# Kernel tuning notes

Measured on AMD Instinct MI355X. Metric: run time of the kernel, lower is better.

The kernel has to match this reference:

```python
import jax, jax.numpy as jnp
import numpy as np

B, C, N, H = 4, 256, 1024, 8
D = C // H
EPS = 1e-5

def setup_inputs() -> dict:
    key = jax.random.key(0)
    ks = jax.random.split(key, 10)
    s = lambda k, shape: (jax.random.normal(k, shape, jnp.float32) * 0.02)
    return dict(
        node_embeds=jax.random.normal(ks[0], (B, C, N), jnp.float32),
        edge_embeds=jax.random.normal(ks[1], (B, N, N), jnp.float32),
        da_prior=jax.random.normal(ks[2], (B, N, C), jnp.float32),
        gamma=jnp.ones((C,), jnp.float32),
        beta=jnp.zeros((C,), jnp.float32),
        w_qkv=s(ks[3], (C, 3 * C)),            # Linear(node_dim, 3*node_dim), no bias
        w_proj=s(ks[4], (C, C)),
        b_proj=jnp.zeros((C,), jnp.float32),
        w_expand=s(ks[5], (H,)),               # Conv2d(1,H,1) weight (per-head scalar)
        b_expand=jnp.zeros((H,), jnp.float32),
        w_reduce=s(ks[6], (H,)),               # Conv2d(H,1,1) weight
        b_reduce=jnp.zeros((1,), jnp.float32),
        w_fc=s(ks[7], (1, C)),                 # Linear(edge_dim=1, node_dim)
        b_fc=jnp.zeros((C,), jnp.float32),
    )

def reference(node_embeds, edge_embeds, da_prior, gamma, beta, w_qkv,
              w_proj, b_proj, w_expand, b_expand, w_reduce, b_reduce, w_fc, b_fc):
    x = jnp.swapaxes(node_embeds, 1, 2)                       # [B,N,C]
    # einsum 'bnn,bnc->bnc': diagonal of edge matrix scales each node
    diag = jnp.diagonal(edge_embeds, axis1=1, axis2=2)        # [B,N]
    attned = diag[:, :, None] * x                             # [B,N,C]
    # einsum 'bnc,bca->bnc' with prior permuted [B,C,A]: multiply by sum over A
    prior_sum = da_prior.sum(axis=1)                          # [B,C]
    x = attned * prior_sum[:, None, :] + x                    # residual add
    # LayerNorm over channel dim
    mu = x.mean(-1, keepdims=True)
    var = x.var(-1, keepdims=True)
    ln = (x - mu) * jax.lax.rsqrt(var + EPS) * gamma + beta
    qkv = (ln @ w_qkv).reshape(B, N, 3, H, D)
    q = jnp.transpose(qkv[:, :, 0], (0, 2, 1, 3))             # [B,H,N,D]
    k = jnp.transpose(qkv[:, :, 1], (0, 2, 1, 3))
    v = jnp.transpose(qkv[:, :, 2], (0, 2, 1, 3))
    scale = D ** -0.5
    attn = jnp.einsum('bhnd,bhmd->bhnm', q, k) * scale        # [B,H,N,N]
    bias = edge_embeds[:, None] * w_expand[None, :, None, None] + b_expand[None, :, None, None]
    attn = attn + bias                                        # pre-softmax scores = residual
    a = jax.nn.softmax(attn, axis=-1)
    node = jnp.einsum('bhnm,bhmd->bnhd', a, v).reshape(B, N, C)
    # reduce conv over heads on (softmax + residual)
    edge = jnp.einsum('bhnm,h->bnm', a + attn, w_reduce) + b_reduce[0]  # [B,N,N]
    w = jax.nn.softmax(edge, axis=-1)
    wsum = (w * edge).sum(-1)                                 # [B,N]
    node = node + wsum[:, :, None] @ w_fc + b_fc              # fc: [B,N,1]@[1,C]
    node = node @ w_proj + b_proj
    return jnp.swapaxes(node, 1, 2), edge                     # ([B,C,N], [B,N,N])
```

## Files before the change

kernel.cpp:

```cpp
#include <hip/hip_runtime.h>
#include <math.h>

#define Bn 4
#define Cn 256
#define Nn 1024
#define Hn 8
#define Dn 32
#define BHND (Bn * Hn * Nn * Dn)
#define BHN  (Bn * Hn * Nn)

typedef short bf16x8 __attribute__((ext_vector_type(8)));
typedef float f32x4 __attribute__((ext_vector_type(4)));

__device__ inline unsigned f2bf_rn_bits(float x) {
  union { float f; unsigned u; } v; v.f = x;
  return (v.u + 0x7FFFu + ((v.u >> 16) & 1u)) >> 16;
}
__device__ inline float bfbits2f(unsigned b) {
  union { unsigned u; float f; } v; v.u = b << 16; return v.f;
}
__device__ inline void split_bf(float x, unsigned& hi, unsigned& lo) {
  hi = f2bf_rn_bits(x);
  lo = f2bf_rn_bits(x - bfbits2f(hi));
}
__device__ inline unsigned split_bf_trunc_pack(float x) {
  union { float f; unsigned u; } v; v.f = x;
  unsigned hi = v.u >> 16;
  union { unsigned u; float f; } hv; hv.u = hi << 16;
  union { float f; unsigned u; } r; r.f = x - hv.f;
  return hi | (r.u & 0xffff0000u);
}
__device__ inline void unpack_u32x8(const uint4& a, const uint4& b, bf16x8& hi, bf16x8& lo) {
  int4 h4, l4;
  h4.x = (int)((a.x & 0xffffu) | (a.y << 16));  l4.x = (int)((a.x >> 16) | (a.y & 0xffff0000u));
  h4.y = (int)((a.z & 0xffffu) | (a.w << 16));  l4.y = (int)((a.z >> 16) | (a.w & 0xffff0000u));
  h4.z = (int)((b.x & 0xffffu) | (b.y << 16));  l4.z = (int)((b.x >> 16) | (b.y & 0xffff0000u));
  h4.w = (int)((b.z & 0xffffu) | (b.w << 16));  l4.w = (int)((b.z >> 16) | (b.w & 0xffff0000u));
  hi = *(bf16x8*)&h4; lo = *(bf16x8*)&l4;
}

__global__ __launch_bounds__(256) void k_pre(const float* __restrict__ w,
                                             const float* __restrict__ dap,
                                             short* __restrict__ wt_h,
                                             short* __restrict__ wt_l,
                                             float* __restrict__ pp) {
  __shared__ float tile[32][33];
  int bi = blockIdx.x;
  if (bi < 32) {
    int b = bi >> 3, ch = bi & 7;
    int c = threadIdx.x;
    float s = 0.f;
    int n0 = ch * 128;
    for (int n = n0; n < n0 + 128; ++n) s += dap[(size_t)(b * Nn + n) * Cn + c];
    pp[(size_t)bi * Cn + c] = s;
  } else {
    int wi = bi - 32;
    int j0 = (wi >> 3) << 5;
    int k0 = (wi & 7) << 5;
    int tx = threadIdx.x & 31, ty = threadIdx.x >> 5;
#pragma unroll
    for (int i = 0; i < 4; ++i)
      tile[ty + i * 8][tx] = w[(size_t)(k0 + ty + i * 8) * 768 + j0 + tx];
    __syncthreads();
#pragma unroll
    for (int i = 0; i < 4; ++i) {
      float v = tile[tx][ty + i * 8];
      unsigned hb, lb; split_bf(v, hb, lb);
      wt_h[(size_t)(j0 + ty + i * 8) * 256 + k0 + tx] = (short)hb;
      wt_l[(size_t)(j0 + ty + i * 8) * 256 + k0 + tx] = (short)lb;
    }
  }
}

__global__ __launch_bounds__(256) void k_prep_ln(const float* __restrict__ ne,
                                                 const float* __restrict__ eg,
                                                 const float* __restrict__ pp,
                                                 const float* __restrict__ gamma,
                                                 const float* __restrict__ beta,
                                                 short* __restrict__ ln_h,
                                                 short* __restrict__ ln_l) {
  int bn = blockIdx.x;
  int b = bn >> 10, n = bn & 1023;
  int c = threadIdx.x;
  float x = ne[(size_t)(b * Cn + c) * Nn + n];
  float pr = 0.f;
#pragma unroll
  for (int ch = 0; ch < 8; ++ch) pr += pp[(size_t)(b * 8 + ch) * Cn + c];
  float dg = eg[(size_t)(b * Nn + n) * Nn + n];
  float x2 = x * (1.f + dg * pr);
  float s = x2, qq = x2 * x2;
#pragma unroll
  for (int off = 32; off >= 1; off >>= 1) {
    s += __shfl_xor(s, off);
    qq += __shfl_xor(qq, off);
  }
  __shared__ float ss[4], sq[4];
  if ((c & 63) == 0) { ss[c >> 6] = s; sq[c >> 6] = qq; }
  __syncthreads();
  s = ss[0] + ss[1] + ss[2] + ss[3];
  qq = sq[0] + sq[1] + sq[2] + sq[3];
  float mu = s * (1.f / 256.f);
  float var = qq * (1.f / 256.f) - mu * mu;
  float r = rsqrtf(var + 1e-5f);
  float v = (x2 - mu) * r * gamma[c] + beta[c];
  unsigned hb, lb; split_bf(v, hb, lb);
  ln_h[(size_t)bn * Cn + c] = (short)hb;
  ln_l[(size_t)bn * Cn + c] = (short)lb;
}

__global__ __launch_bounds__(256) void k_qkv_mfma(
    const short* __restrict__ ln_h, const short* __restrict__ ln_l,
    const short* __restrict__ wt_h, const short* __restrict__ wt_l,
    short* __restrict__ q_hi, short* __restrict__ q_lo,
    short* __restrict__ k_hi, short* __restrict__ k_lo,
    short* __restrict__ vt_hi, short* __restrict__ vt_lo) {
  __shared__ float ct[64][65];
  int m0 = blockIdx.x * 64;
  int j0 = blockIdx.y * 64;
  int t = threadIdx.x, wid = t >> 6, l = t & 63;
  int lr = l & 15, lq = l >> 4;
  f32x4 acc[4] = {};
  const short* ah_p = ln_h + (size_t)(m0 + wid * 16 + lr) * 256 + lq * 8;
  const short* al_p = ln_l + (size_t)(m0 + wid * 16 + lr) * 256 + lq * 8;
  const short* bh_p = wt_h + (size_t)(j0 + lr) * 256 + lq * 8;
  const short* bl_p = wt_l + (size_t)(j0 + lr) * 256 + lq * 8;
#pragma unroll 2
  for (int k0 = 0; k0 < 256; k0 += 32) {
    bf16x8 ah = *(const bf16x8*)&ah_p[k0];
    bf16x8 al = *(const bf16x8*)&al_p[k0];
#pragma unroll
    for (int js = 0; js < 4; ++js) {
      bf16x8 bh = *(const bf16x8*)&bh_p[js * 16 * 256 + k0];
      bf16x8 bl = *(const bf16x8*)&bl_p[js * 16 * 256 + k0];
      acc[js] = __builtin_amdgcn_mfma_f32_16x16x32_bf16(al, bh, acc[js], 0, 0, 0);
      acc[js] = __builtin_amdgcn_mfma_f32_16x16x32_bf16(ah, bl, acc[js], 0, 0, 0);
      acc[js] = __builtin_amdgcn_mfma_f32_16x16x32_bf16(ah, bh, acc[js], 0, 0, 0);
    }
  }
#pragma unroll
  for (int js = 0; js < 4; ++js)
#pragma unroll
    for (int reg = 0; reg < 4; ++reg)
      ct[wid * 16 + lq * 4 + reg][js * 16 + lr] = acc[js][reg];
  __syncthreads();
  int b = m0 >> 10, n0 = m0 & 1023;
  int three = j0 >> 8;
  const float scale = 0.17677669529663687f;
  if (three == 2) {
    int jl = t >> 2;
    int n4 = (t & 3) * 16;
    int rem = (j0 & 255) + jl;
    int h = rem >> 5, d = rem & 31;
    short hs[16], ls[16];
#pragma unroll
    for (int u = 0; u < 16; ++u) {
      unsigned hb, lb;
      split_bf(ct[n4 + u][jl], hb, lb);
      hs[u] = (short)hb; ls[u] = (short)lb;
    }
    size_t ob = ((size_t)(b * Hn + h) * Dn + d) * Nn + n0 + n4;
    *(uint4*)&vt_hi[ob] = *(uint4*)&hs[0];
    *(uint4*)&vt_hi[ob + 8] = *(uint4*)&hs[8];
    *(uint4*)&vt_lo[ob] = *(uint4*)&ls[0];
    *(uint4*)&vt_lo[ob + 8] = *(uint4*)&ls[8];
  } else {
    int m_l = t & 63, half = t >> 6;
    int rem = (j0 & 255) + half * 16;
    int h = rem >> 5, ddb = rem & 31;
    int n = n0 + m_l;
    float sc = (three == 0) ? 1.0f : scale;
    short* dh = three ? k_hi : q_hi;
    short* dl = three ? k_lo : q_lo;
    short hs[16], ls[16];
#pragma unroll
    for (int u = 0; u < 16; ++u) {
      unsigned hb, lb;
      split_bf(ct[m_l][half * 16 + u] * sc, hb, lb);
      hs[u] = (short)hb; ls[u] = (short)lb;
    }
    size_t base = ((size_t)((b * Hn + h) * Nn + n)) * Dn + ddb;
    *(uint4*)&dh[base] = *(uint4*)&hs[0];
    *(uint4*)&dh[base + 8] = *(uint4*)&hs[8];
    *(uint4*)&dl[base] = *(uint4*)&ls[0];
    *(uint4*)&dl[base + 8] = *(uint4*)&ls[8];
  }
}

__global__ __launch_bounds__(256, 4) void k_attn_core(
    const short* __restrict__ q_hi, const short* __restrict__ q_lo,
    const short* __restrict__ k_hi, const short* __restrict__ k_lo,
    const short* __restrict__ vt_hi, const short* __restrict__ vt_lo,
    const float* __restrict__ eg,
    const float* __restrict__ w_expand, const float* __restrict__ b_expand,
    float* __restrict__ o_part, float* __restrict__ l_part) {
  __shared__ short kh[64 * 40];
  __shared__ short kl[64 * 40];
  __shared__ short vth[32 * 72];
  __shared__ short vtl[32 * 72];
  __shared__ unsigned pbuf[4][16 * 68];

  int blk = blockIdx.x;
  int mh = blk & 1;
  int nt = (blk >> 1) & 15;
  int h = (blk >> 5) & 7;
  int b = blk >> 8;
  int n0 = nt * 64;
  int t = threadIdx.x, wid = t >> 6, l = t & 63;
  int lr = l & 15, lq = l >> 4;

  const float we = w_expand[h], be = b_expand[h];
  size_t bhb = (size_t)(b * Hn + h) * Nn * Dn;
  const short* khg = k_hi + bhb;
  const short* klg = k_lo + bhb;
  const short* vhg = vt_hi + bhb;
  const short* vlg = vt_lo + bhb;

  bf16x8 qhi, qlo;
  {
    size_t qoff = bhb + (size_t)(n0 + wid * 16 + lr) * Dn + lq * 8;
    qhi = *(const bf16x8*)&q_hi[qoff];
    qlo = *(const bf16x8*)&q_lo[qoff];
  }

  f32x4 O0 = {0.f, 0.f, 0.f, 0.f}, O1 = {0.f, 0.f, 0.f, 0.f};
  float rowsum[4] = {0.f, 0.f, 0.f, 0.f};
  int nrow = n0 + wid * 16 + lq * 4;

  for (int ms = 0; ms < 8; ++ms) {
    int m0 = mh * 512 + ms * 64;
    float eb[4][4];
#pragma unroll
    for (int reg = 0; reg < 4; ++reg) {
      const float* ep = &eg[(size_t)(b * Nn + nrow + reg) * Nn + m0 + lr];
#pragma unroll
      for (int msub = 0; msub < 4; ++msub) eb[msub][reg] = ep[msub * 16];
    }
    __syncthreads();
    {
      int row = t >> 2, c = (t & 3) * 8;
      *(uint4*)&kh[row * 40 + c] = *(const uint4*)&khg[(size_t)(m0 + row) * Dn + c];
      *(uint4*)&kl[row * 40 + c] = *(const uint4*)&klg[(size_t)(m0 + row) * Dn + c];
      int d = t >> 3, cm = (t & 7) * 8;
      *(uint4*)&vth[d * 72 + cm] = *(const uint4*)&vhg[(size_t)d * Nn + m0 + cm];
      *(uint4*)&vtl[d * 72 + cm] = *(const uint4*)&vlg[(size_t)d * Nn + m0 + cm];
    }
    __syncthreads();

#pragma unroll
    for (int msub = 0; msub < 4; ++msub) {
      int mrow = msub * 16 + lr;
      bf16x8 bh8 = *(bf16x8*)&kh[mrow * 40 + lq * 8];
      bf16x8 bl8 = *(bf16x8*)&kl[mrow * 40 + lq * 8];
      f32x4 sacc = {0.f, 0.f, 0.f, 0.f};
      sacc = __builtin_amdgcn_mfma_f32_16x16x32_bf16(qlo, bh8, sacc, 0, 0, 0);
      sacc = __builtin_amdgcn_mfma_f32_16x16x32_bf16(qhi, bl8, sacc, 0, 0, 0);
      sacc = __builtin_amdgcn_mfma_f32_16x16x32_bf16(qhi, bh8, sacc, 0, 0, 0);
#pragma unroll
      for (int reg = 0; reg < 4; ++reg) {
        float s = sacc[reg] + eb[msub][reg] * we + be;
        float e = __expf(s);
        rowsum[reg] += e;
        pbuf[wid][(lq * 4 + reg) * 68 + msub * 16 + lr] = split_bf_trunc_pack(e);
      }
    }

#pragma unroll
    for (int mw = 0; mw < 2; ++mw) {
      uint4 pa = *(uint4*)&pbuf[wid][lr * 68 + mw * 32 + lq * 8];
      uint4 pb = *(uint4*)&pbuf[wid][lr * 68 + mw * 32 + lq * 8 + 4];
      bf16x8 ahi, alo;
      unpack_u32x8(pa, pb, ahi, alo);
      {
        bf16x8 vh8 = *(bf16x8*)&vth[lr * 72 + mw * 32 + lq * 8];
        bf16x8 vl8 = *(bf16x8*)&vtl[lr * 72 + mw * 32 + lq * 8];
        O0 = __builtin_amdgcn_mfma_f32_16x16x32_bf16(alo, vh8, O0, 0, 0, 0);
        O0 = __builtin_amdgcn_mfma_f32_16x16x32_bf16(ahi, vl8, O0, 0, 0, 0);
        O0 = __builtin_amdgcn_mfma_f32_16x16x32_bf16(ahi, vh8, O0, 0, 0, 0);
      }
      {
        bf16x8 vh8 = *(bf16x8*)&vth[(16 + lr) * 72 + mw * 32 + lq * 8];
        bf16x8 vl8 = *(bf16x8*)&vtl[(16 + lr) * 72 + mw * 32 + lq * 8];
        O1 = __builtin_amdgcn_mfma_f32_16x16x32_bf16(alo, vh8, O1, 0, 0, 0);
        O1 = __builtin_amdgcn_mfma_f32_16x16x32_bf16(ahi, vl8, O1, 0, 0, 0);
        O1 = __builtin_amdgcn_mfma_f32_16x16x32_bf16(ahi, vh8, O1, 0, 0, 0);
      }
    }
  }

#pragma unroll
  for (int reg = 0; reg < 4; ++reg) {
#pragma unroll
    for (int off = 1; off < 16; off <<= 1)
      rowsum[reg] += __shfl_xor(rowsum[reg], off);
  }
  size_t pbase = (size_t)mh * BHND + bhb;
#pragma unroll
  for (int reg = 0; reg < 4; ++reg) {
    int n = nrow + reg;
    o_part[pbase + (size_t)n * Dn + lr] = O0[reg];
    o_part[pbase + (size_t)n * Dn + 16 + lr] = O1[reg];
    if (lr == 0)
      l_part[(size_t)mh * BHN + (size_t)(b * Hn + h) * Nn + n] = rowsum[reg];
  }
}

__global__ __launch_bounds__(256, 4) void k_edge_mfma(
    const short* __restrict__ q_hi, const short* __restrict__ q_lo,
    const short* __restrict__ k_hi, const short* __restrict__ k_lo,
    const float* __restrict__ eg, const float* __restrict__ l_part,
    const float* __restrict__ w_expand, const float* __restrict__ b_expand,
    const float* __restrict__ w_reduce, const float* __restrict__ b_reduce,
    float* __restrict__ edge_out, float* __restrict__ pl_part,
    float* __restrict__ pwe_part) {
  __shared__ short kh[64 * 40];
  __shared__ short kl[64 * 40];
  int blk = blockIdx.x;
  int mt = blk & 15;
  int nt = (blk >> 4) & 15;
  int b = blk >> 8;
  int n0 = nt * 64, m0 = mt * 64;
  int t = threadIdx.x, wid = t >> 6, l = t & 63;
  int lr = l & 15, lq = l >> 4;
  const float br = b_reduce[0];
  int nrow = n0 + wid * 16 + lq * 4;

  float eacc[4][4], ebias[4][4];
#pragma unroll
  for (int reg = 0; reg < 4; ++reg) {
    const float* ep = &eg[(size_t)(b * Nn + nrow + reg) * Nn + m0 + lr];
#pragma unroll
    for (int msub = 0; msub < 4; ++msub) {
      ebias[msub][reg] = ep[msub * 16];
      eacc[msub][reg] = br;
    }
  }

  for (int h = 0; h < Hn; ++h) {
    size_t bhb = (size_t)(b * Hn + h) * Nn * Dn;
    float we = w_expand[h], be = b_expand[h], wr = w_reduce[h];
    bf16x8 qhi, qlo;
    {
      size_t qoff = bhb + (size_t)(n0 + wid * 16 + lr) * Dn + lq * 8;
      qhi = *(const bf16x8*)&q_hi[qoff];
      qlo = *(const bf16x8*)&q_lo[qoff];
    }
    float invl[4];
#pragma unroll
    for (int reg = 0; reg < 4; ++reg) {
      size_t idx = (size_t)(b * Hn + h) * Nn + nrow + reg;
      invl[reg] = 1.0f / (l_part[idx] + l_part[BHN + idx]);
    }

    __syncthreads();
    {
      int row = t >> 2, c = (t & 3) * 8;
      *(uint4*)&kh[row * 40 + c] = *(const uint4*)&k_hi[bhb + (size_t)(m0 + row) * Dn + c];
      *(uint4*)&kl[row * 40 + c] = *(const uint4*)&k_lo[bhb + (size_t)(m0 + row) * Dn + c];
    }
    __syncthreads();
#pragma unroll
    for (int msub = 0; msub < 4; ++msub) {
      int mrow = msub * 16 + lr;
      bf16x8 bh8 = *(bf16x8*)&kh[mrow * 40 + lq * 8];
      bf16x8 bl8 = *(bf16x8*)&kl[mrow * 40 + lq * 8];
      f32x4 sacc = {0.f, 0.f, 0.f, 0.f};
      sacc = __builtin_amdgcn_mfma_f32_16x16x32_bf16(qlo, bh8, sacc, 0, 0, 0);
      sacc = __builtin_amdgcn_mfma_f32_16x16x32_bf16(qhi, bl8, sacc, 0, 0, 0);
      sacc = __builtin_amdgcn_mfma_f32_16x16x32_bf16(qhi, bh8, sacc, 0, 0, 0);
#pragma unroll
      for (int reg = 0; reg < 4; ++reg) {
        float s = sacc[reg] + ebias[msub][reg] * we + be;
        float p = __expf(s) * invl[reg];
        eacc[msub][reg] += wr * (p + s);
      }
    }
  }
#pragma unroll
  for (int msub = 0; msub < 4; ++msub)
#pragma unroll
    for (int reg = 0; reg < 4; ++reg)
      edge_out[(size_t)(b * Nn + nrow + reg) * Nn + m0 + msub * 16 + lr] = eacc[msub][reg];

  float pl[4] = {0.f, 0.f, 0.f, 0.f}, pw[4] = {0.f, 0.f, 0.f, 0.f};
#pragma unroll
  for (int msub = 0; msub < 4; ++msub)
#pragma unroll
    for (int reg = 0; reg < 4; ++reg) {
      float e = eacc[msub][reg];
      float x = __expf(e);
      pl[reg] += x;
      pw[reg] += x * e;
    }
#pragma unroll
  for (int reg = 0; reg < 4; ++reg) {
#pragma unroll
    for (int off = 1; off < 16; off <<= 1) {
      pl[reg] += __shfl_xor(pl[reg], off);
      pw[reg] += __shfl_xor(pw[reg], off);
    }
    if (lr == 0) {
      int idx = mt * (Bn * Nn) + b * Nn + nrow + reg;
      pl_part[idx] = pl[reg];
      pwe_part[idx] = pw[reg];
    }
  }
}

__global__ __launch_bounds__(256) void k_proj_gemm(const float* __restrict__ o_part,
                                                   const float* __restrict__ l_part,
                                                   const float* __restrict__ pl,
                                                   const float* __restrict__ pwe,
                                                   const float* __restrict__ wfc,
                                                   const float* __restrict__ bfc,
                                                   const float* __restrict__ wproj,
                                                   const float* __restrict__ bproj,
                                                   float* __restrict__ out) {
  __shared__ __align__(16) float at[16][68];
  __shared__ __align__(16) float bt[16][68];
  __shared__ float ct[64][65];
  __shared__ float wsm_s[64];
  int m0 = blockIdx.x * 64;
  int j0 = blockIdx.y * 64;
  int t = threadIdx.x;
  int tx = t & 15, ty = t >> 4;
  if (t < 64) {
    int m = m0 + t;
    float L = 0.f, Wv = 0.f;
#pragma unroll
    for (int mt = 0; mt < 16; ++mt) {
      L += pl[mt * (Bn * Nn) + m];
      Wv += pwe[mt * (Bn * Nn) + m];
    }
    wsm_s[t] = Wv / L;
  }
  __syncthreads();
  float4 acc[4] = {};
  for (int k0 = 0; k0 < 256; k0 += 16) {
    {
      int row = t >> 2, k4 = (t & 3) << 2;
      int m = m0 + row;
      int bb = m >> 10, n = m & 1023;
      int c = k0 + k4;
      int h = c >> 5, dd = c & 31;
      float wsm = wsm_s[row];
      size_t ob = ((size_t)(bb * Hn + h) * Nn + n) * Dn + dd;
      float4 oa = *(const float4*)&o_part[ob];
      float4 oc = *(const float4*)&o_part[BHND + ob];
      size_t sidx = (size_t)(bb * Hn + h) * Nn + n;
      float inv = 1.0f / (l_part[sidx] + l_part[BHN + sidx]);
      float4 a;
      a.x = (oa.x + oc.x) * inv + wsm * wfc[c + 0] + bfc[c + 0];
      a.y = (oa.y + oc.y) * inv + wsm * wfc[c + 1] + bfc[c + 1];
      a.z = (oa.z + oc.z) * inv + wsm * wfc[c + 2] + bfc[c + 2];
      a.w = (oa.w + oc.w) * inv + wsm * wfc[c + 3] + bfc[c + 3];
      at[k4 + 0][row] = a.x; at[k4 + 1][row] = a.y;
      at[k4 + 2][row] = a.z; at[k4 + 3][row] = a.w;
      int rb = t >> 4, jb = (t & 15) << 2;
      *(float4*)&bt[rb][jb] = *(const float4*)&wproj[(size_t)(k0 + rb) * 256 + j0 + jb];
    }
    __syncthreads();
#pragma unroll
    for (int kk = 0; kk < 16; ++kk) {
      float4 a4 = *(float4*)&at[kk][ty << 2];
      float4 b4 = *(float4*)&bt[kk][tx << 2];
      acc[0].x += a4.x * b4.x; acc[0].y += a4.x * b4.y; acc[0].z += a4.x * b4.z; acc[0].w += a4.x * b4.w;
      acc[1].x += a4.y * b4.x; acc[1].y += a4.y * b4.y; acc[1].z += a4.y * b4.z; acc[1].w += a4.y * b4.w;
      acc[2].x += a4.z * b4.x; acc[2].y += a4.z * b4.y; acc[2].z += a4.z * b4.z; acc[2].w += a4.z * b4.w;
      acc[3].x += a4.w * b4.x; acc[3].y += a4.w * b4.y; acc[3].z += a4.w * b4.z; acc[3].w += a4.w * b4.w;
    }
    __syncthreads();
  }
#pragma unroll
  for (int i = 0; i < 4; ++i) {
    ct[(ty << 2) + i][(tx << 2) + 0] = acc[i].x + bproj[j0 + (tx << 2) + 0];
    ct[(ty << 2) + i][(tx << 2) + 1] = acc[i].y + bproj[j0 + (tx << 2) + 1];
    ct[(ty << 2) + i][(tx << 2) + 2] = acc[i].z + bproj[j0 + (tx << 2) + 2];
    ct[(ty << 2) + i][(tx << 2) + 3] = acc[i].w + bproj[j0 + (tx << 2) + 3];
  }
  __syncthreads();
  int b = m0 >> 10, n0 = m0 & 1023;
  int n4 = t & 15, c0i = t >> 4;
#pragma unroll
  for (int u = 0; u < 4; ++u) {
    int ci = c0i + u * 16;
    float4 val = { ct[(n4 << 2) + 0][ci], ct[(n4 << 2) + 1][ci],
                   ct[(n4 << 2) + 2][ci], ct[(n4 << 2) + 3][ci] };
    *(float4*)&out[(size_t)(b * Cn + j0 + ci) * Nn + n0 + (n4 << 2)] = val;
  }
}

extern "C" void kernel_launch(void* const* d_in, const int* in_sizes, int n_in,
                              void* d_out, int out_size, void* d_ws, size_t ws_size,
                              hipStream_t stream) {
  (void)in_sizes; (void)n_in; (void)out_size; (void)ws_size;
  const float* node_embeds = (const float*)d_in[0];
  const float* edge_embeds = (const float*)d_in[1];
  const float* da_prior    = (const float*)d_in[2];
  const float* gamma       = (const float*)d_in[3];
  const float* beta        = (const float*)d_in[4];
  const float* w_qkv       = (const float*)d_in[5];
  const float* w_proj      = (const float*)d_in[6];
  const float* b_proj      = (const float*)d_in[7];
  const float* w_expand    = (const float*)d_in[8];
  const float* b_expand    = (const float*)d_in[9];
  const float* w_reduce    = (const float*)d_in[10];
  const float* b_reduce    = (const float*)d_in[11];
  const float* w_fc        = (const float*)d_in[12];
  const float* b_fc        = (const float*)d_in[13];
  float* out_node = (float*)d_out;
  float* out_edge = out_node + (size_t)Bn * Cn * Nn;

  const size_t M = 1048576;
  float* W = (float*)d_ws;
  short* ln_hi  = (short*)(W + M);
  short* ln_lo  = ln_hi + M;
  float* o_part = W;
  short* vt_hi  = (short*)(W + 2 * M);
  short* vt_lo  = vt_hi + M;
  short* q_hi   = (short*)(W + 3 * M);
  short* q_lo   = q_hi + M;
  short* k_hi   = q_hi + 2 * M;
  short* k_lo   = q_hi + 3 * M;
  float* ws_pp    = W + 5 * M;
  float* l_part   = ws_pp + Bn * 8 * Cn;
  float* pl_part  = l_part + 2 * BHN;
  float* pwe_part = pl_part + 16 * Bn * Nn;
  short* wt_hi    = (short*)(pwe_part + 16 * Bn * Nn);
  short* wt_lo    = wt_hi + 768 * 256;

  k_pre<<<dim3(224), dim3(256), 0, stream>>>(w_qkv, da_prior, wt_hi, wt_lo, ws_pp);
  k_prep_ln<<<dim3(Bn * Nn), dim3(256), 0, stream>>>(node_embeds, edge_embeds, ws_pp,
                                                     gamma, beta, ln_hi, ln_lo);
  k_qkv_mfma<<<dim3(64, 12), dim3(256), 0, stream>>>(ln_hi, ln_lo, wt_hi, wt_lo,
                                                     q_hi, q_lo, k_hi, k_lo,
                                                     vt_hi, vt_lo);
  k_attn_core<<<dim3(Bn * Hn * 16 * 2), dim3(256), 0, stream>>>(
      q_hi, q_lo, k_hi, k_lo, vt_hi, vt_lo, edge_embeds, w_expand, b_expand,
      o_part, l_part);
  k_edge_mfma<<<dim3(Bn * 16 * 16), dim3(256), 0, stream>>>(
      q_hi, q_lo, k_hi, k_lo, edge_embeds, l_part, w_expand, b_expand,
      w_reduce, b_reduce, out_edge, pl_part, pwe_part);
  k_proj_gemm<<<dim3(64, 4), dim3(256), 0, stream>>>(o_part, l_part, pl_part,
                                                     pwe_part, w_fc, b_fc,
                                                     w_proj, b_proj, out_node);
}
```

Before: 202.2 us.

## Stage QKV GEMM tiles in LDS and process two heads per attention block

The QKV GEMM now loads its A and B hi/lo tiles cooperatively into shared memory, prefetching the next k-slice into registers, so per-wave global loads of B are no longer repeated across waves. The attention core kernel now handles two heads per block, so each edge-bias tile read from global memory is reused for both heads. This halves the grid, relaxes launch bounds to 2 blocks per SM, and doubles per-block register state. The cost is fewer blocks for latency hiding and extra syncs.

```diff
diff --git a/kernel.cpp b/kernel.cpp
--- a/kernel.cpp
+++ b/kernel.cpp
@@ -114,29 +114,49 @@
     short* __restrict__ q_hi, short* __restrict__ q_lo,
     short* __restrict__ k_hi, short* __restrict__ k_lo,
     short* __restrict__ vt_hi, short* __restrict__ vt_lo) {
+  __shared__ short Ah[64 * 40];
+  __shared__ short Al[64 * 40];
+  __shared__ short Bh[64 * 40];
+  __shared__ short Bl[64 * 40];
   __shared__ float ct[64][65];
   int m0 = blockIdx.x * 64;
   int j0 = blockIdx.y * 64;
   int t = threadIdx.x, wid = t >> 6, l = t & 63;
   int lr = l & 15, lq = l >> 4;
   f32x4 acc[4] = {};
-  const short* ah_p = ln_h + (size_t)(m0 + wid * 16 + lr) * 256 + lq * 8;
-  const short* al_p = ln_l + (size_t)(m0 + wid * 16 + lr) * 256 + lq * 8;
-  const short* bh_p = wt_h + (size_t)(j0 + lr) * 256 + lq * 8;
-  const short* bl_p = wt_l + (size_t)(j0 + lr) * 256 + lq * 8;
-#pragma unroll 2
-  for (int k0 = 0; k0 < 256; k0 += 32) {
-    bf16x8 ah = *(const bf16x8*)&ah_p[k0];
-    bf16x8 al = *(const bf16x8*)&al_p[k0];
+  int row = t >> 2, ch = (t & 3) * 8;
+  const short* a_h_src = ln_h + (size_t)(m0 + row) * 256 + ch;
+  const short* a_l_src = ln_l + (size_t)(m0 + row) * 256 + ch;
+  const short* b_h_src = wt_h + (size_t)(j0 + row) * 256 + ch;
+  const short* b_l_src = wt_l + (size_t)(j0 + row) * 256 + ch;
+  uint4 vah = *(const uint4*)&a_h_src[0];
+  uint4 val = *(const uint4*)&a_l_src[0];
+  uint4 vbh = *(const uint4*)&b_h_src[0];
+  uint4 vbl = *(const uint4*)&b_l_src[0];
+  for (int it = 0; it < 8; ++it) {
+    __syncthreads();
+    *(uint4*)&Ah[row * 40 + ch] = vah;
+    *(uint4*)&Al[row * 40 + ch] = val;
+    *(uint4*)&Bh[row * 40 + ch] = vbh;
+    *(uint4*)&Bl[row * 40 + ch] = vbl;
+    __syncthreads();
+    int kn = ((it + 1) & 7) * 32;
+    vah = *(const uint4*)&a_h_src[kn];
+    val = *(const uint4*)&a_l_src[kn];
+    vbh = *(const uint4*)&b_h_src[kn];
+    vbl = *(const uint4*)&b_l_src[kn];
+    bf16x8 ah = *(bf16x8*)&Ah[(wid * 16 + lr) * 40 + lq * 8];
+    bf16x8 al8 = *(bf16x8*)&Al[(wid * 16 + lr) * 40 + lq * 8];
 #pragma unroll
     for (int js = 0; js < 4; ++js) {
-      bf16x8 bh = *(const bf16x8*)&bh_p[js * 16 * 256 + k0];
-      bf16x8 bl = *(const bf16x8*)&bl_p[js * 16 * 256 + k0];
-      acc[js] = __builtin_amdgcn_mfma_f32_16x16x32_bf16(al, bh, acc[js], 0, 0, 0);
+      bf16x8 bh = *(bf16x8*)&Bh[(js * 16 + lr) * 40 + lq * 8];
+      bf16x8 bl = *(bf16x8*)&Bl[(js * 16 + lr) * 40 + lq * 8];
+      acc[js] = __builtin_amdgcn_mfma_f32_16x16x32_bf16(al8, bh, acc[js], 0, 0, 0);
       acc[js] = __builtin_amdgcn_mfma_f32_16x16x32_bf16(ah, bl, acc[js], 0, 0, 0);
       acc[js] = __builtin_amdgcn_mfma_f32_16x16x32_bf16(ah, bh, acc[js], 0, 0, 0);
     }
   }
+  __syncthreads();
 #pragma unroll
   for (int js = 0; js < 4; ++js)
 #pragma unroll
@@ -186,7 +206,7 @@
   }
 }
 
-__global__ __launch_bounds__(256, 4) void k_attn_core(
+__global__ __launch_bounds__(256, 2) void k_attn_core(
     const short* __restrict__ q_hi, const short* __restrict__ q_lo,
     const short* __restrict__ k_hi, const short* __restrict__ k_lo,
     const short* __restrict__ vt_hi, const short* __restrict__ vt_lo,
@@ -202,28 +222,28 @@
   int blk = blockIdx.x;
   int mh = blk & 1;
   int nt = (blk >> 1) & 15;
-  int h = (blk >> 5) & 7;
-  int b = blk >> 8;
+  int hp = (blk >> 5) & 3;
+  int b = blk >> 7;
   int n0 = nt * 64;
   int t = threadIdx.x, wid = t >> 6, l = t & 63;
   int lr = l & 15, lq = l >> 4;
 
-  const float we = w_expand[h], be = b_expand[h];
-  size_t bhb = (size_t)(b * Hn + h) * Nn * Dn;
-  const short* khg = k_hi + bhb;
-  const short* klg = k_lo + bhb;
-  const short* vhg = vt_hi + bhb;
-  const short* vlg = vt_lo + bhb;
-
-  bf16x8 qhi, qlo;
-  {
-    size_t qoff = bhb + (size_t)(n0 + wid * 16 + lr) * Dn + lq * 8;
-    qhi = *(const bf16x8*)&q_hi[qoff];
-    qlo = *(const bf16x8*)&q_lo[qoff];
-  }
-
-  f32x4 O0 = {0.f, 0.f, 0.f, 0.f}, O1 = {0.f, 0.f, 0.f, 0.f};
-  float rowsum[4] = {0.f, 0.f, 0.f, 0.f};
+  float we[2], be[2];
+  size_t bhb[2];
+  bf16x8 qhi[2], qlo[2];
+#pragma unroll
+  for (int hh = 0; hh < 2; ++hh) {
+    int h = hp * 2 + hh;
+    we[hh] = w_expand[h]; be[hh] = b_expand[h];
+    bhb[hh] = (size_t)(b * Hn + h) * Nn * Dn;
+    size_t qoff = bhb[hh] + (size_t)(n0 + wid * 16 + lr) * Dn + lq * 8;
+    qhi[hh] = *(const bf16x8*)&q_hi[qoff];
+    qlo[hh] = *(const bf16x8*)&q_lo[qoff];
+  }
+
+  f32x4 O0[2] = {{0.f,0.f,0.f,0.f},{0.f,0.f,0.f,0.f}};
+  f32x4 O1[2] = {{0.f,0.f,0.f,0.f},{0.f,0.f,0.f,0.f}};
+  float rowsum[2][4] = {};
   int nrow = n0 + wid * 16 + lq * 4;
 
   for (int ms = 0; ms < 8; ++ms) {
@@ -235,72 +255,82 @@
 #pragma unroll
       for (int msub = 0; msub < 4; ++msub) eb[msub][reg] = ep[msub * 16];
     }
-    __syncthreads();
-    {
-      int row = t >> 2, c = (t & 3) * 8;
-      *(uint4*)&kh[row * 40 + c] = *(const uint4*)&khg[(size_t)(m0 + row) * Dn + c];
-      *(uint4*)&kl[row * 40 + c] = *(const uint4*)&klg[(size_t)(m0 + row) * Dn + c];
-      int d = t >> 3, cm = (t & 7) * 8;
-      *(uint4*)&vth[d * 72 + cm] = *(const uint4*)&vhg[(size_t)d * Nn + m0 + cm];
-      *(uint4*)&vtl[d * 72 + cm] = *(const uint4*)&vlg[(size_t)d * Nn + m0 + cm];
-    }
-    __syncthreads();
-
-#pragma unroll
-    for (int msub = 0; msub < 4; ++msub) {
-      int mrow = msub * 16 + lr;
-      bf16x8 bh8 = *(bf16x8*)&kh[mrow * 40 + lq * 8];
-      bf16x8 bl8 = *(bf16x8*)&kl[mrow * 40 + lq * 8];
-      f32x4 sacc = {0.f, 0.f, 0.f, 0.f};
-      sacc = __builtin_amdgcn_mfma_f32_16x16x32_bf16(qlo, bh8, sacc, 0, 0, 0);
-      sacc = __builtin_amdgcn_mfma_f32_16x16x32_bf16(qhi, bl8, sacc, 0, 0, 0);
-      sacc = __builtin_amdgcn_mfma_f32_16x16x32_bf16(qhi, bh8, sacc, 0, 0, 0);
-#pragma unroll
-      for (int reg = 0; reg < 4; ++reg) {
-        float s = sacc[reg] + eb[msub][reg] * we + be;
-        float e = __expf(s);
-        rowsum[reg] += e;
-        pbuf[wid][(lq * 4 + reg) * 68 + msub * 16 + lr] = split_bf_trunc_pack(e);
+#pragma unroll
+    for (int hh = 0; hh < 2; ++hh) {
+      __syncthreads();
+      {
+        int row = t >> 2, c = (t & 3) * 8;
+        const short* khg = k_hi + bhb[hh];
+        const short* klg = k_lo + bhb[hh];
+        const short* vhg = vt_hi + bhb[hh];
+        const short* vlg = vt_lo + bhb[hh];
+        *(uint4*)&kh[row * 40 + c] = *(const uint4*)&khg[(size_t)(m0 + row) * Dn + c];
+        *(uint4*)&kl[row * 40 + c] = *(const uint4*)&klg[(size_t)(m0 + row) * Dn + c];
+        int d = t >> 3, cm = (t & 7) * 8;
+        *(uint4*)&vth[d * 72 + cm] = *(const uint4*)&vhg[(size_t)d * Nn + m0 + cm];
+        *(uint4*)&vtl[d * 72 + cm] = *(const uint4*)&vlg[(size_t)d * Nn + m0 + cm];
       }
-    }
-
-#pragma unroll
-    for (int mw = 0; mw < 2; ++mw) {
-      uint4 pa = *(uint4*)&pbuf[wid][lr * 68 + mw * 32 + lq * 8];
-      uint4 pb = *(uint4*)&pbuf[wid][lr * 68 + mw * 32 + lq * 8 + 4];
-      bf16x8 ahi, alo;
-      unpack_u32x8(pa, pb, ahi, alo);
-      {
-        bf16x8 vh8 = *(bf16x8*)&vth[lr * 72 + mw * 32 + lq * 8];
-        bf16x8 vl8 = *(bf16x8*)&vtl[lr * 72 + mw * 32 + lq * 8];
-        O0 = __builtin_amdgcn_mfma_f32_16x16x32_bf16(alo, vh8, O0, 0, 0, 0);
-        O0 = __builtin_amdgcn_mfma_f32_16x16x32_bf16(ahi, vl8, O0, 0, 0, 0);
-        O0 = __builtin_amdgcn_mfma_f32_16x16x32_bf16(ahi, vh8, O0, 0, 0, 0);
+      __syncthreads();
+
+#pragma unroll
+      for (int msub = 0; msub < 4; ++msub) {
+        int mrow = msub * 16 + lr;
+        bf16x8 bh8 = *(bf16x8*)&kh[mrow * 40 + lq * 8];
+        bf16x8 bl8 = *(bf16x8*)&kl[mrow * 40 + lq * 8];
+        f32x4 sacc = {0.f, 0.f, 0.f, 0.f};
+        sacc = __builtin_amdgcn_mfma_f32_16x16x32_bf16(qlo[hh], bh8, sacc, 0, 0, 0);
+        sacc = __builtin_amdgcn_mfma_f32_16x16x32_bf16(qhi[hh], bl8, sacc, 0, 0, 0);
+        sacc = __builtin_amdgcn_mfma_f32_16x16x32_bf16(qhi[hh], bh8, sacc, 0, 0, 0);
+#pragma unroll
+        for (int reg = 0; reg < 4; ++reg) {
+          float s = sacc[reg] + eb[msub][reg] * we[hh] + be[hh];
+          float e = __expf(s);
+          rowsum[hh][reg] += e;
+          pbuf[wid][(lq * 4 + reg) * 68 + msub * 16 + lr] = split_bf_trunc_pack(e);
+        }
       }
-      {
-        bf16x8 vh8 = *(bf16x8*)&vth[(16 + lr) * 72 + mw * 32 + lq * 8];
-        bf16x8 vl8 = *(bf16x8*)&vtl[(16 + lr) * 72 + mw * 32 + lq * 8];
-        O1 = __builtin_amdgcn_mfma_f32_16x16x32_bf16(alo, vh8, O1, 0, 0, 0);
-        O1 = __builtin_amdgcn_mfma_f32_16x16x32_bf16(ahi, vl8, O1, 0, 0, 0);
-        O1 = __builtin_amdgcn_mfma_f32_16x16x32_bf16(ahi, vh8, O1, 0, 0, 0);
+
+#pragma unroll
+      for (int mw = 0; mw < 2; ++mw) {
+        uint4 pa = *(uint4*)&pbuf[wid][lr * 68 + mw * 32 + lq * 8];
+        uint4 pb = *(uint4*)&pbuf[wid][lr * 68 + mw * 32 + lq * 8 + 4];
+        bf16x8 ahi, alo;
+        unpack_u32x8(pa, pb, ahi, alo);
+        {
+          bf16x8 vh8 = *(bf16x8*)&vth[lr * 72 + mw * 32 + lq * 8];
+          bf16x8 vl8 = *(bf16x8*)&vtl[lr * 72 + mw * 32 + lq * 8];
+          O0[hh] = __builtin_amdgcn_mfma_f32_16x16x32_bf16(alo, vh8, O0[hh], 0, 0, 0);
+          O0[hh] = __builtin_amdgcn_mfma_f32_16x16x32_bf16(ahi, vl8, O0[hh], 0, 0, 0);
+          O0[hh] = __builtin_amdgcn_mfma_f32_16x16x32_bf16(ahi, vh8, O0[hh], 0, 0, 0);
+        }
+        {
+          bf16x8 vh8 = *(bf16x8*)&vth[(16 + lr) * 72 + mw * 32 + lq * 8];
+          bf16x8 vl8 = *(bf16x8*)&vtl[(16 + lr) * 72 + mw * 32 + lq * 8];
+          O1[hh] = __builtin_amdgcn_mfma_f32_16x16x32_bf16(alo, vh8, O1[hh], 0, 0, 0);
+          O1[hh] = __builtin_amdgcn_mfma_f32_16x16x32_bf16(ahi, vl8, O1[hh], 0, 0, 0);
+          O1[hh] = __builtin_amdgcn_mfma_f32_16x16x32_bf16(ahi, vh8, O1[hh], 0, 0, 0);
+        }
       }
     }
   }
 
 #pragma unroll
-  for (int reg = 0; reg < 4; ++reg) {
-#pragma unroll
-    for (int off = 1; off < 16; off <<= 1)
-      rowsum[reg] += __shfl_xor(rowsum[reg], off);
-  }
-  size_t pbase = (size_t)mh * BHND + bhb;
-#pragma unroll
-  for (int reg = 0; reg < 4; ++reg) {
-    int n = nrow + reg;
-    o_part[pbase + (size_t)n * Dn + lr] = O0[reg];
-    o_part[pbase + (size_t)n * Dn + 16 + lr] = O1[reg];
-    if (lr == 0)
-      l_part[(size_t)mh * BHN + (size_t)(b * Hn + h) * Nn + n] = rowsum[reg];
+  for (int hh = 0; hh < 2; ++hh) {
+#pragma unroll
+    for (int reg = 0; reg < 4; ++reg) {
+#pragma unroll
+      for (int off = 1; off < 16; off <<= 1)
+        rowsum[hh][reg] += __shfl_xor(rowsum[hh][reg], off);
+    }
+    size_t pbase = (size_t)mh * BHND + bhb[hh];
+#pragma unroll
+    for (int reg = 0; reg < 4; ++reg) {
+      int n = nrow + reg;
+      o_part[pbase + (size_t)n * Dn + lr] = O0[hh][reg];
+      o_part[pbase + (size_t)n * Dn + 16 + lr] = O1[hh][reg];
+      if (lr == 0)
+        l_part[(size_t)mh * BHN + (size_t)(b * Hn + hp * 2 + hh) * Nn + n] = rowsum[hh][reg];
+    }
   }
 }
 
@@ -534,7 +564,7 @@
   k_qkv_mfma<<<dim3(64, 12), dim3(256), 0, stream>>>(ln_hi, ln_lo, wt_hi, wt_lo,
                                                      q_hi, q_lo, k_hi, k_lo,
                                                      vt_hi, vt_lo);
-  k_attn_core<<<dim3(Bn * Hn * 16 * 2), dim3(256), 0, stream>>>(
+  k_attn_core<<<dim3(Bn * 4 * 16 * 2), dim3(256), 0, stream>>>(
       q_hi, q_lo, k_hi, k_lo, vt_hi, vt_lo, edge_embeds, w_expand, b_expand,
       o_part, l_part);
   k_edge_mfma<<<dim3(Bn * 16 * 16), dim3(256), 0, stream>>>(
```

Measured after the change: 202.6 us. No clear change (+0.2%).

## Register-prefetch next K/V tiles and stage QKV GEMM operands through LDS

Applied to the files above, without the earlier changes.

The QKV projection kernel now loads A and B tiles into shared memory cooperatively, prefetching the next k-slice into registers while the current one is consumed by MFMA. The attention and edge kernels prefetch the next K (and V) tile into registers before computing on the current LDS tile, so global loads overlap with compute. This trades extra registers, LDS and barriers for better latency hiding and fewer redundant global loads.

```diff
diff --git a/kernel.cpp b/kernel.cpp
--- a/kernel.cpp
+++ b/kernel.cpp
@@ -114,29 +114,49 @@
     short* __restrict__ q_hi, short* __restrict__ q_lo,
     short* __restrict__ k_hi, short* __restrict__ k_lo,
     short* __restrict__ vt_hi, short* __restrict__ vt_lo) {
+  __shared__ short Ah[64 * 40];
+  __shared__ short Al[64 * 40];
+  __shared__ short Bh[64 * 40];
+  __shared__ short Bl[64 * 40];
   __shared__ float ct[64][65];
   int m0 = blockIdx.x * 64;
   int j0 = blockIdx.y * 64;
   int t = threadIdx.x, wid = t >> 6, l = t & 63;
   int lr = l & 15, lq = l >> 4;
   f32x4 acc[4] = {};
-  const short* ah_p = ln_h + (size_t)(m0 + wid * 16 + lr) * 256 + lq * 8;
-  const short* al_p = ln_l + (size_t)(m0 + wid * 16 + lr) * 256 + lq * 8;
-  const short* bh_p = wt_h + (size_t)(j0 + lr) * 256 + lq * 8;
-  const short* bl_p = wt_l + (size_t)(j0 + lr) * 256 + lq * 8;
-#pragma unroll 2
-  for (int k0 = 0; k0 < 256; k0 += 32) {
-    bf16x8 ah = *(const bf16x8*)&ah_p[k0];
-    bf16x8 al = *(const bf16x8*)&al_p[k0];
+  int row = t >> 2, ch = (t & 3) * 8;
+  const short* a_h_src = ln_h + (size_t)(m0 + row) * 256 + ch;
+  const short* a_l_src = ln_l + (size_t)(m0 + row) * 256 + ch;
+  const short* b_h_src = wt_h + (size_t)(j0 + row) * 256 + ch;
+  const short* b_l_src = wt_l + (size_t)(j0 + row) * 256 + ch;
+  uint4 vah = *(const uint4*)&a_h_src[0];
+  uint4 val = *(const uint4*)&a_l_src[0];
+  uint4 vbh = *(const uint4*)&b_h_src[0];
+  uint4 vbl = *(const uint4*)&b_l_src[0];
+  for (int it = 0; it < 8; ++it) {
+    __syncthreads();
+    *(uint4*)&Ah[row * 40 + ch] = vah;
+    *(uint4*)&Al[row * 40 + ch] = val;
+    *(uint4*)&Bh[row * 40 + ch] = vbh;
+    *(uint4*)&Bl[row * 40 + ch] = vbl;
+    __syncthreads();
+    int kn = ((it + 1) & 7) * 32;
+    vah = *(const uint4*)&a_h_src[kn];
+    val = *(const uint4*)&a_l_src[kn];
+    vbh = *(const uint4*)&b_h_src[kn];
+    vbl = *(const uint4*)&b_l_src[kn];
+    bf16x8 ah = *(bf16x8*)&Ah[(wid * 16 + lr) * 40 + lq * 8];
+    bf16x8 al8 = *(bf16x8*)&Al[(wid * 16 + lr) * 40 + lq * 8];
 #pragma unroll
     for (int js = 0; js < 4; ++js) {
-      bf16x8 bh = *(const bf16x8*)&bh_p[js * 16 * 256 + k0];
-      bf16x8 bl = *(const bf16x8*)&bl_p[js * 16 * 256 + k0];
-      acc[js] = __builtin_amdgcn_mfma_f32_16x16x32_bf16(al, bh, acc[js], 0, 0, 0);
+      bf16x8 bh = *(bf16x8*)&Bh[(js * 16 + lr) * 40 + lq * 8];
+      bf16x8 bl = *(bf16x8*)&Bl[(js * 16 + lr) * 40 + lq * 8];
+      acc[js] = __builtin_amdgcn_mfma_f32_16x16x32_bf16(al8, bh, acc[js], 0, 0, 0);
       acc[js] = __builtin_amdgcn_mfma_f32_16x16x32_bf16(ah, bl, acc[js], 0, 0, 0);
       acc[js] = __builtin_amdgcn_mfma_f32_16x16x32_bf16(ah, bh, acc[js], 0, 0, 0);
     }
   }
+  __syncthreads();
 #pragma unroll
   for (int js = 0; js < 4; ++js)
 #pragma unroll
@@ -222,6 +242,17 @@
     qlo = *(const bf16x8*)&q_lo[qoff];
   }
 
+  int srow = t >> 2, sc = (t & 3) * 8;
+  int sd = t >> 3, scm = (t & 7) * 8;
+  uint4 rkh, rkl, rvh, rvl;
+  {
+    int m0 = mh * 512;
+    rkh = *(const uint4*)&khg[(size_t)(m0 + srow) * Dn + sc];
+    rkl = *(const uint4*)&klg[(size_t)(m0 + srow) * Dn + sc];
+    rvh = *(const uint4*)&vhg[(size_t)sd * Nn + m0 + scm];
+    rvl = *(const uint4*)&vlg[(size_t)sd * Nn + m0 + scm];
+  }
+
   f32x4 O0 = {0.f, 0.f, 0.f, 0.f}, O1 = {0.f, 0.f, 0.f, 0.f};
   float rowsum[4] = {0.f, 0.f, 0.f, 0.f};
   int nrow = n0 + wid * 16 + lq * 4;
@@ -236,15 +267,18 @@
       for (int msub = 0; msub < 4; ++msub) eb[msub][reg] = ep[msub * 16];
     }
     __syncthreads();
+    *(uint4*)&kh[srow * 40 + sc] = rkh;
+    *(uint4*)&kl[srow * 40 + sc] = rkl;
+    *(uint4*)&vth[sd * 72 + scm] = rvh;
+    *(uint4*)&vtl[sd * 72 + scm] = rvl;
+    __syncthreads();
     {
-      int row = t >> 2, c = (t & 3) * 8;
-      *(uint4*)&kh[row * 40 + c] = *(const uint4*)&khg[(size_t)(m0 + row) * Dn + c];
-      *(uint4*)&kl[row * 40 + c] = *(const uint4*)&klg[(size_t)(m0 + row) * Dn + c];
-      int d = t >> 3, cm = (t & 7) * 8;
-      *(uint4*)&vth[d * 72 + cm] = *(const uint4*)&vhg[(size_t)d * Nn + m0 + cm];
-      *(uint4*)&vtl[d * 72 + cm] = *(const uint4*)&vlg[(size_t)d * Nn + m0 + cm];
-    }
-    __syncthreads();
+      int mn0 = mh * 512 + ((ms < 7) ? ms + 1 : ms) * 64;
+      rkh = *(const uint4*)&khg[(size_t)(mn0 + srow) * Dn + sc];
+      rkl = *(const uint4*)&klg[(size_t)(mn0 + srow) * Dn + sc];
+      rvh = *(const uint4*)&vhg[(size_t)sd * Nn + mn0 + scm];
+      rvl = *(const uint4*)&vlg[(size_t)sd * Nn + mn0 + scm];
+    }
 
 #pragma unroll
     for (int msub = 0; msub < 4; ++msub) {
@@ -335,6 +369,14 @@
     }
   }
 
+  int srow = t >> 2, sc = (t & 3) * 8;
+  uint4 rkh, rkl;
+  {
+    size_t bhb0 = (size_t)(b * Hn) * Nn * Dn;
+    rkh = *(const uint4*)&k_hi[bhb0 + (size_t)(m0 + srow) * Dn + sc];
+    rkl = *(const uint4*)&k_lo[bhb0 + (size_t)(m0 + srow) * Dn + sc];
+  }
+
   for (int h = 0; h < Hn; ++h) {
     size_t bhb = (size_t)(b * Hn + h) * Nn * Dn;
     float we = w_expand[h], be = b_expand[h], wr = w_reduce[h];
@@ -352,12 +394,14 @@
     }
 
     __syncthreads();
+    *(uint4*)&kh[srow * 40 + sc] = rkh;
+    *(uint4*)&kl[srow * 40 + sc] = rkl;
+    __syncthreads();
     {
-      int row = t >> 2, c = (t & 3) * 8;
-      *(uint4*)&kh[row * 40 + c] = *(const uint4*)&k_hi[bhb + (size_t)(m0 + row) * Dn + c];
-      *(uint4*)&kl[row * 40 + c] = *(const uint4*)&k_lo[bhb + (size_t)(m0 + row) * Dn + c];
-    }
-    __syncthreads();
+      size_t bhn = (size_t)(b * Hn + ((h < 7) ? h + 1 : h)) * Nn * Dn;
+      rkh = *(const uint4*)&k_hi[bhn + (size_t)(m0 + srow) * Dn + sc];
+      rkl = *(const uint4*)&k_lo[bhn + (size_t)(m0 + srow) * Dn + sc];
+    }
 #pragma unroll
     for (int msub = 0; msub < 4; ++msub) {
       int mrow = msub * 16 + lr;
```

After: 185.6 us. -8.2%, faster.
